# Performance work log

Hardware: AMD Instinct MI355X
Metric: run time of the kernel (lower is better)

Reference implementation:

```python
import jax, jax.numpy as jnp
import numpy as np
from jax.scipy.special import logsumexp

EXPERT_NUM = 64
MOE_TOPK = 2

def setup_inputs() -> dict:
    key = jax.random.key(0)
    k1, k2 = jax.random.split(key)
    x = jax.random.normal(k1, (4, 4096, 4096), dtype=jnp.float32)
    # nn.Linear(input_size, expert_num).weight has shape [expert_num, input_size]
    W = jax.random.normal(k2, (EXPERT_NUM, 4096), dtype=jnp.float32) * (1.0 / np.sqrt(4096))
    return {"x": x, "W": W}

def reference(x, W):
    # logits: [B, S, E]
    logits = jnp.einsum('bsd,ed->bse', x, W)
    k = min(MOE_TOPK + 1, EXPERT_NUM)  # torch takes topk+1 then slices
    topk_logits, topk_indices = jax.lax.top_k(logits, k)
    topk_logits = topk_logits[..., :MOE_TOPK]     # [B, S, K]
    topk_indices = topk_indices[..., :MOE_TOPK]   # [B, S, K]
    # regularized=True: softmax over the top-k logits in float32
    topk_scores = jax.nn.softmax(topk_logits.astype(jnp.float32), axis=-1).astype(logits.dtype)
    # scatter into zeros; topk indices are unique so one-hot sum == scatter-set
    scores_filtered = jnp.sum(
        jax.nn.one_hot(topk_indices, EXPERT_NUM, dtype=logits.dtype) * topk_scores[..., None],
        axis=-2)  # [B, S, E]
    # router_z loss, per-token [B, S]
    log_z = logsumexp(logits, axis=-1)
    loss = log_z ** 2
    return logits, scores_filtered, loss
```

## Files before the change

kernel.cpp:

```cpp
#include <hip/hip_runtime.h>
#include <math.h>

#define TTOK 16384
#define DD   4096
#define EE   64
#define TM   64
#define BK   64
#define NCH  (DD / BK)
#define XSTR 72

typedef __attribute__((ext_vector_type(8))) short short8;
typedef __attribute__((ext_vector_type(4))) float f32x4;

static __device__ __forceinline__ unsigned short f2bf(float f) {
    unsigned u = __float_as_uint(f);
    u += 0x7FFFu + ((u >> 16) & 1u);
    return (unsigned short)(u >> 16);
}
static __device__ __forceinline__ float bf2f(unsigned short h) {
    return __uint_as_float(((unsigned)h) << 16);
}

__global__ __launch_bounds__(256, 1)
void moe_gate_mfma(const float* __restrict__ x,
                   const float* __restrict__ W,
                   float* __restrict__ out)
{
    __shared__ unsigned short stage[4 * TM * XSTR];
    __shared__ float s1a[TM], s2a[TM];
    __shared__ int   i1a[TM], i2a[TM];

    unsigned short* const xh = stage;
    unsigned short* const xl = stage + 1 * TM * XSTR;
    unsigned short* const wh = stage + 2 * TM * XSTR;
    unsigned short* const wl = stage + 3 * TM * XSTR;

    const int tid  = threadIdx.x;
    const int t0   = blockIdx.x * TM;
    const int r    = tid >> 4;
    const int c4   = (tid & 15) * 4;
    const int w    = tid >> 6;
    const int lane = tid & 63;
    const int m    = lane & 15;
    const int q    = lane >> 4;

    f32x4 acc[4];
#pragma unroll
    for (int e = 0; e < 4; ++e) acc[e] = (f32x4){0.f, 0.f, 0.f, 0.f};

    float4 xr[4], wr[4];
#pragma unroll
    for (int p = 0; p < 4; ++p) {
        const int row = 16 * p + r;
        xr[p] = *reinterpret_cast<const float4*>(x + (size_t)(t0 + row) * DD + c4);
        wr[p] = *reinterpret_cast<const float4*>(W + (size_t)row * DD + c4);
    }

    const unsigned short* const aHp = xh + (16 * w + m) * XSTR + q * 8;
    const unsigned short* const aLp = xl + (16 * w + m) * XSTR + q * 8;
    const unsigned short* const bHp = wh + m * XSTR + q * 8;
    const unsigned short* const bLp = wl + m * XSTR + q * 8;

    for (int kc = 0; kc < NCH; ++kc) {
        __syncthreads();
#pragma unroll
        for (int p = 0; p < 4; ++p) {
            const int row = 16 * p + r;
            float4 v = xr[p];
            ushort4 h, l;
            h.x = f2bf(v.x); h.y = f2bf(v.y); h.z = f2bf(v.z); h.w = f2bf(v.w);
            l.x = f2bf(v.x - bf2f(h.x)); l.y = f2bf(v.y - bf2f(h.y));
            l.z = f2bf(v.z - bf2f(h.z)); l.w = f2bf(v.w - bf2f(h.w));
            *reinterpret_cast<ushort4*>(xh + row * XSTR + c4) = h;
            *reinterpret_cast<ushort4*>(xl + row * XSTR + c4) = l;
            v = wr[p];
            h.x = f2bf(v.x); h.y = f2bf(v.y); h.z = f2bf(v.z); h.w = f2bf(v.w);
            l.x = f2bf(v.x - bf2f(h.x)); l.y = f2bf(v.y - bf2f(h.y));
            l.z = f2bf(v.z - bf2f(h.z)); l.w = f2bf(v.w - bf2f(h.w));
            *reinterpret_cast<ushort4*>(wh + row * XSTR + c4) = h;
            *reinterpret_cast<ushort4*>(wl + row * XSTR + c4) = l;
        }
        __syncthreads();

        if (kc + 1 < NCH) {
            const int off = (kc + 1) * BK + c4;
#pragma unroll
            for (int p = 0; p < 4; ++p) {
                const int row = 16 * p + r;
                xr[p] = *reinterpret_cast<const float4*>(x + (size_t)(t0 + row) * DD + off);
                wr[p] = *reinterpret_cast<const float4*>(W + (size_t)row * DD + off);
            }
        }

#pragma unroll
        for (int ks = 0; ks < 2; ++ks) {
            const short8 ah = *reinterpret_cast<const short8*>(aHp + ks * 32);
            const short8 al = *reinterpret_cast<const short8*>(aLp + ks * 32);
#pragma unroll
            for (int e = 0; e < 4; ++e) {
                const short8 bh = *reinterpret_cast<const short8*>(bHp + e * 16 * XSTR + ks * 32);
                const short8 bl = *reinterpret_cast<const short8*>(bLp + e * 16 * XSTR + ks * 32);
                acc[e] = __builtin_amdgcn_mfma_f32_16x16x32_bf16(ah, bh, acc[e], 0, 0, 0);
                acc[e] = __builtin_amdgcn_mfma_f32_16x16x32_bf16(ah, bl, acc[e], 0, 0, 0);
                acc[e] = __builtin_amdgcn_mfma_f32_16x16x32_bf16(al, bh, acc[e], 0, 0, 0);
            }
        }
    }

    __syncthreads();
    float* lg = reinterpret_cast<float*>(stage);

#pragma unroll
    for (int e = 0; e < 4; ++e) {
#pragma unroll
        for (int i = 0; i < 4; ++i) {
            lg[(16 * w + 4 * q + i) * 65 + 16 * e + m] = acc[e][i];
        }
    }
    __syncthreads();

    if (tid < TM) {
        const int t = tid;
        const float* row = lg + t * 65;
        float v1 = -INFINITY, v2 = -INFINITY;
        int   i1 = 0, i2 = 0;
        for (int e = 0; e < EE; ++e) {
            const float v = row[e];
            if (v > v1)      { v2 = v1; i2 = i1; v1 = v; i1 = e; }
            else if (v > v2) { v2 = v;  i2 = e; }
        }
        float s = 0.f;
        for (int e = 0; e < EE; ++e) s += expf(row[e] - v1);
        const float logz = v1 + logf(s);
        out[(size_t)2 * TTOK * EE + t0 + t] = logz * logz;
        const float e21 = expf(v2 - v1);
        const float rr  = 1.f / (1.f + e21);
        s1a[t] = rr; s2a[t] = e21 * rr; i1a[t] = i1; i2a[t] = i2;
    }
    __syncthreads();

    float* sc = out + (size_t)TTOK * EE;
    const int ty = tid >> 4;
    const int tx = tid & 15;
#pragma unroll
    for (int i = 0; i < 4; ++i) {
        const int tok = 4 * ty + i;
        const float* row = lg + tok * 65 + 4 * tx;
        *reinterpret_cast<float4*>(out + (size_t)(t0 + tok) * EE + 4 * tx) =
            make_float4(row[0], row[1], row[2], row[3]);
        const int i1 = i1a[tok], i2 = i2a[tok];
        const float s1 = s1a[tok], s2 = s2a[tok];
        float vv[4];
#pragma unroll
        for (int j = 0; j < 4; ++j) {
            const int e = 4 * tx + j;
            vv[j] = (e == i1) ? s1 : ((e == i2) ? s2 : 0.f);
        }
        *reinterpret_cast<float4*>(sc + (size_t)(t0 + tok) * EE + 4 * tx) =
            make_float4(vv[0], vv[1], vv[2], vv[3]);
    }
}

extern "C" void kernel_launch(void* const* d_in, const int* in_sizes, int n_in,
                              void* d_out, int out_size, void* d_ws, size_t ws_size,
                              hipStream_t stream) {
    const float* x = (const float*)d_in[0];
    const float* W = (const float*)d_in[1];
    float* out = (float*)d_out;
    moe_gate_mfma<<<dim3(TTOK / TM), dim3(256), 0, stream>>>(x, W, out);
}
```

Before: 402.3 us.

## Pre-convert W to bf16 hi/lo and split K across waves without LDS staging

A separate kernel first converts W into bf16 hi/lo arrays in workspace, so each block no longer re-splits W per tile. The main kernel drops LDS staging and the per-chunk barriers. Each wave loads its x fragments straight from global memory into registers and owns a quarter of the K dimension for a 32-token tile. The partial sums are reduced through LDS at the end. This cuts conversion work and synchronisation and allows two blocks per CU, at the cost of uncoalesced direct global loads of W fragments and an extra kernel launch.

```diff
diff --git a/kernel.cpp b/kernel.cpp
--- a/kernel.cpp
+++ b/kernel.cpp
@@ -4,10 +4,10 @@
 #define TTOK 16384
 #define DD   4096
 #define EE   64
-#define TM   64
-#define BK   64
-#define NCH  (DD / BK)
-#define XSTR 72
+#define TMB  32
+#define KW   1024
+#define NIT  (KW / 32)
+#define PST  68
 
 typedef __attribute__((ext_vector_type(8))) short short8;
 typedef __attribute__((ext_vector_type(4))) float f32x4;
@@ -21,107 +21,125 @@
     return __uint_as_float(((unsigned)h) << 16);
 }
 
-__global__ __launch_bounds__(256, 1)
-void moe_gate_mfma(const float* __restrict__ x,
-                   const float* __restrict__ W,
-                   float* __restrict__ out)
+static __device__ __forceinline__ void cvt8(float4 a, float4 b, short8& hi, short8& lo) {
+    const float v[8] = {a.x, a.y, a.z, a.w, b.x, b.y, b.z, b.w};
+#pragma unroll
+    for (int j = 0; j < 8; ++j) {
+        const unsigned short h = f2bf(v[j]);
+        hi[j] = (short)h;
+        lo[j] = (short)f2bf(v[j] - bf2f(h));
+    }
+}
+
+__global__ void w_convert(const float* __restrict__ W,
+                          unsigned short* __restrict__ whi,
+                          unsigned short* __restrict__ wlo) {
+    const int i = (blockIdx.x * blockDim.x + threadIdx.x) * 4;
+    if (i >= EE * DD) return;
+    const float4 v = *reinterpret_cast<const float4*>(W + i);
+    ushort4 h, l;
+    h.x = f2bf(v.x); l.x = f2bf(v.x - bf2f(h.x));
+    h.y = f2bf(v.y); l.y = f2bf(v.y - bf2f(h.y));
+    h.z = f2bf(v.z); l.z = f2bf(v.z - bf2f(h.z));
+    h.w = f2bf(v.w); l.w = f2bf(v.w - bf2f(h.w));
+    *reinterpret_cast<ushort4*>(whi + i) = h;
+    *reinterpret_cast<ushort4*>(wlo + i) = l;
+}
+
+__global__ __launch_bounds__(256, 2)
+void moe_gate_v3(const float* __restrict__ x,
+                 const unsigned short* __restrict__ whi,
+                 const unsigned short* __restrict__ wlo,
+                 float* __restrict__ out)
 {
-    __shared__ unsigned short stage[4 * TM * XSTR];
-    __shared__ float s1a[TM], s2a[TM];
-    __shared__ int   i1a[TM], i2a[TM];
-
-    unsigned short* const xh = stage;
-    unsigned short* const xl = stage + 1 * TM * XSTR;
-    unsigned short* const wh = stage + 2 * TM * XSTR;
-    unsigned short* const wl = stage + 3 * TM * XSTR;
+    __shared__ float ps[4 * TMB * PST];
+    __shared__ float s1a[TMB], s2a[TMB];
+    __shared__ int   i1a[TMB], i2a[TMB];
 
     const int tid  = threadIdx.x;
-    const int t0   = blockIdx.x * TM;
-    const int r    = tid >> 4;
-    const int c4   = (tid & 15) * 4;
-    const int w    = tid >> 6;
+    const int wv   = tid >> 6;
     const int lane = tid & 63;
     const int m    = lane & 15;
     const int q    = lane >> 4;
+    const int t0   = blockIdx.x * TMB;
 
-    f32x4 acc[4];
+    const int kq = wv * KW + q * 8;
+    const float*          xp0 = x   + (size_t)(t0 + m) * DD + kq;
+    const float*          xp1 = xp0 + (size_t)16 * DD;
+    const unsigned short* whp = whi + (size_t)m * DD + kq;
+    const unsigned short* wlp = wlo + (size_t)m * DD + kq;
+
+    f32x4 acc[2][4];
 #pragma unroll
-    for (int e = 0; e < 4; ++e) acc[e] = (f32x4){0.f, 0.f, 0.f, 0.f};
+    for (int mi = 0; mi < 2; ++mi)
+#pragma unroll
+        for (int e = 0; e < 4; ++e) acc[mi][e] = (f32x4){0.f, 0.f, 0.f, 0.f};
 
-    float4 xr[4], wr[4];
+    float4 a0 = *reinterpret_cast<const float4*>(xp0);
+    float4 a1 = *reinterpret_cast<const float4*>(xp0 + 4);
+    float4 a2 = *reinterpret_cast<const float4*>(xp1);
+    float4 a3 = *reinterpret_cast<const float4*>(xp1 + 4);
+
+    for (int it = 0; it < NIT; ++it) {
+        float4 n0, n1, n2, n3;
+        if (it + 1 < NIT) {
+            const float* p0 = xp0 + (it + 1) * 32;
+            const float* p1 = xp1 + (it + 1) * 32;
+            n0 = *reinterpret_cast<const float4*>(p0);
+            n1 = *reinterpret_cast<const float4*>(p0 + 4);
+            n2 = *reinterpret_cast<const float4*>(p1);
+            n3 = *reinterpret_cast<const float4*>(p1 + 4);
+        }
+        short8 ah0, al0, ah1, al1;
+        cvt8(a0, a1, ah0, al0);
+        cvt8(a2, a3, ah1, al1);
 #pragma unroll
-    for (int p = 0; p < 4; ++p) {
-        const int row = 16 * p + r;
-        xr[p] = *reinterpret_cast<const float4*>(x + (size_t)(t0 + row) * DD + c4);
-        wr[p] = *reinterpret_cast<const float4*>(W + (size_t)row * DD + c4);
+        for (int e = 0; e < 4; ++e) {
+            const short8 bh = *reinterpret_cast<const short8*>(whp + (size_t)e * 16 * DD + it * 32);
+            const short8 bl = *reinterpret_cast<const short8*>(wlp + (size_t)e * 16 * DD + it * 32);
+            acc[0][e] = __builtin_amdgcn_mfma_f32_16x16x32_bf16(ah0, bh, acc[0][e], 0, 0, 0);
+            acc[0][e] = __builtin_amdgcn_mfma_f32_16x16x32_bf16(ah0, bl, acc[0][e], 0, 0, 0);
+            acc[0][e] = __builtin_amdgcn_mfma_f32_16x16x32_bf16(al0, bh, acc[0][e], 0, 0, 0);
+            acc[1][e] = __builtin_amdgcn_mfma_f32_16x16x32_bf16(ah1, bh, acc[1][e], 0, 0, 0);
+            acc[1][e] = __builtin_amdgcn_mfma_f32_16x16x32_bf16(ah1, bl, acc[1][e], 0, 0, 0);
+            acc[1][e] = __builtin_amdgcn_mfma_f32_16x16x32_bf16(al1, bh, acc[1][e], 0, 0, 0);
+        }
+        a0 = n0; a1 = n1; a2 = n2; a3 = n3;
     }
 
-    const unsigned short* const aHp = xh + (16 * w + m) * XSTR + q * 8;
-    const unsigned short* const aLp = xl + (16 * w + m) * XSTR + q * 8;
-    const unsigned short* const bHp = wh + m * XSTR + q * 8;
-    const unsigned short* const bLp = wl + m * XSTR + q * 8;
+#pragma unroll
+    for (int mi = 0; mi < 2; ++mi)
+#pragma unroll
+        for (int e = 0; e < 4; ++e)
+#pragma unroll
+            for (int i = 0; i < 4; ++i)
+                ps[wv * TMB * PST + (mi * 16 + 4 * q + i) * PST + 16 * e + m] = acc[mi][e][i];
+    __syncthreads();
 
-    for (int kc = 0; kc < NCH; ++kc) {
-        __syncthreads();
+    {
+        const int c0  = tid * 8;
+        const int tok = c0 >> 6;
+        const int e0  = c0 & 63;
+        float* base = ps + tok * PST + e0;
+        float4 s0 = *reinterpret_cast<const float4*>(base);
+        float4 s1 = *reinterpret_cast<const float4*>(base + 4);
 #pragma unroll
-        for (int p = 0; p < 4; ++p) {
-            const int row = 16 * p + r;
-            float4 v = xr[p];
-            ushort4 h, l;
-            h.x = f2bf(v.x); h.y = f2bf(v.y); h.z = f2bf(v.z); h.w = f2bf(v.w);
-            l.x = f2bf(v.x - bf2f(h.x)); l.y = f2bf(v.y - bf2f(h.y));
-            l.z = f2bf(v.z - bf2f(h.z)); l.w = f2bf(v.w - bf2f(h.w));
-            *reinterpret_cast<ushort4*>(xh + row * XSTR + c4) = h;
-            *reinterpret_cast<ushort4*>(xl + row * XSTR + c4) = l;
-            v = wr[p];
-            h.x = f2bf(v.x); h.y = f2bf(v.y); h.z = f2bf(v.z); h.w = f2bf(v.w);
-            l.x = f2bf(v.x - bf2f(h.x)); l.y = f2bf(v.y - bf2f(h.y));
-            l.z = f2bf(v.z - bf2f(h.z)); l.w = f2bf(v.w - bf2f(h.w));
-            *reinterpret_cast<ushort4*>(wh + row * XSTR + c4) = h;
-            *reinterpret_cast<ushort4*>(wl + row * XSTR + c4) = l;
+        for (int w = 1; w < 4; ++w) {
+            const float4 r0 = *reinterpret_cast<const float4*>(base + w * TMB * PST);
+            const float4 r1 = *reinterpret_cast<const float4*>(base + w * TMB * PST + 4);
+            s0.x += r0.x; s0.y += r0.y; s0.z += r0.z; s0.w += r0.w;
+            s1.x += r1.x; s1.y += r1.y; s1.z += r1.z; s1.w += r1.w;
         }
-        __syncthreads();
-
-        if (kc + 1 < NCH) {
-            const int off = (kc + 1) * BK + c4;
-#pragma unroll
-            for (int p = 0; p < 4; ++p) {
-                const int row = 16 * p + r;
-                xr[p] = *reinterpret_cast<const float4*>(x + (size_t)(t0 + row) * DD + off);
-                wr[p] = *reinterpret_cast<const float4*>(W + (size_t)row * DD + off);
-            }
-        }
-
-#pragma unroll
-        for (int ks = 0; ks < 2; ++ks) {
-            const short8 ah = *reinterpret_cast<const short8*>(aHp + ks * 32);
-            const short8 al = *reinterpret_cast<const short8*>(aLp + ks * 32);
-#pragma unroll
-            for (int e = 0; e < 4; ++e) {
-                const short8 bh = *reinterpret_cast<const short8*>(bHp + e * 16 * XSTR + ks * 32);
-                const short8 bl = *reinterpret_cast<const short8*>(bLp + e * 16 * XSTR + ks * 32);
-                acc[e] = __builtin_amdgcn_mfma_f32_16x16x32_bf16(ah, bh, acc[e], 0, 0, 0);
-                acc[e] = __builtin_amdgcn_mfma_f32_16x16x32_bf16(ah, bl, acc[e], 0, 0, 0);
-                acc[e] = __builtin_amdgcn_mfma_f32_16x16x32_bf16(al, bh, acc[e], 0, 0, 0);
-            }
-        }
-    }
-
-    __syncthreads();
-    float* lg = reinterpret_cast<float*>(stage);
-
-#pragma unroll
-    for (int e = 0; e < 4; ++e) {
-#pragma unroll
-        for (int i = 0; i < 4; ++i) {
-            lg[(16 * w + 4 * q + i) * 65 + 16 * e + m] = acc[e][i];
-        }
+        float* g = out + (size_t)(t0 + tok) * EE + e0;
+        *reinterpret_cast<float4*>(g)     = s0;
+        *reinterpret_cast<float4*>(g + 4) = s1;
+        *reinterpret_cast<float4*>(base)     = s0;
+        *reinterpret_cast<float4*>(base + 4) = s1;
     }
     __syncthreads();
 
-    if (tid < TM) {
-        const int t = tid;
-        const float* row = lg + t * 65;
+    if (tid < TMB) {
+        const float* row = ps + tid * PST;
         float v1 = -INFINITY, v2 = -INFINITY;
         int   i1 = 0, i2 = 0;
         for (int e = 0; e < EE; ++e) {
@@ -132,32 +150,29 @@
         float s = 0.f;
         for (int e = 0; e < EE; ++e) s += expf(row[e] - v1);
         const float logz = v1 + logf(s);
-        out[(size_t)2 * TTOK * EE + t0 + t] = logz * logz;
+        out[(size_t)2 * TTOK * EE + t0 + tid] = logz * logz;
         const float e21 = expf(v2 - v1);
         const float rr  = 1.f / (1.f + e21);
-        s1a[t] = rr; s2a[t] = e21 * rr; i1a[t] = i1; i2a[t] = i2;
+        s1a[tid] = rr; s2a[tid] = e21 * rr; i1a[tid] = i1; i2a[tid] = i2;
     }
     __syncthreads();
 
-    float* sc = out + (size_t)TTOK * EE;
-    const int ty = tid >> 4;
-    const int tx = tid & 15;
-#pragma unroll
-    for (int i = 0; i < 4; ++i) {
-        const int tok = 4 * ty + i;
-        const float* row = lg + tok * 65 + 4 * tx;
-        *reinterpret_cast<float4*>(out + (size_t)(t0 + tok) * EE + 4 * tx) =
-            make_float4(row[0], row[1], row[2], row[3]);
+    {
+        float* sc = out + (size_t)TTOK * EE;
+        const int c0  = tid * 8;
+        const int tok = c0 >> 6;
+        const int e0  = c0 & 63;
         const int i1 = i1a[tok], i2 = i2a[tok];
         const float s1 = s1a[tok], s2 = s2a[tok];
-        float vv[4];
+        float vv[8];
 #pragma unroll
-        for (int j = 0; j < 4; ++j) {
-            const int e = 4 * tx + j;
+        for (int j = 0; j < 8; ++j) {
+            const int e = e0 + j;
             vv[j] = (e == i1) ? s1 : ((e == i2) ? s2 : 0.f);
         }
-        *reinterpret_cast<float4*>(sc + (size_t)(t0 + tok) * EE + 4 * tx) =
-            make_float4(vv[0], vv[1], vv[2], vv[3]);
+        float* g = sc + (size_t)(t0 + tok) * EE + e0;
+        *reinterpret_cast<float4*>(g)     = make_float4(vv[0], vv[1], vv[2], vv[3]);
+        *reinterpret_cast<float4*>(g + 4) = make_float4(vv[4], vv[5], vv[6], vv[7]);
     }
 }
 
@@ -167,5 +182,8 @@
     const float* x = (const float*)d_in[0];
     const float* W = (const float*)d_in[1];
     float* out = (float*)d_out;
-    moe_gate_mfma<<<dim3(TTOK / TM), dim3(256), 0, stream>>>(x, W, out);
+    unsigned short* whi = (unsigned short*)d_ws;
+    unsigned short* wlo = whi + (size_t)EE * DD;
+    w_convert<<<dim3((EE * DD / 4 + 255) / 256), dim3(256), 0, stream>>>(W, whi, wlo);
+    moe_gate_v3<<<dim3(TTOK / TMB), dim3(256), 0, stream>>>(x, whi, wlo, out);
 }
```

After: 417.3 us. 1.04x slower.
